# Kernel tuning notes

Measured on AMD Instinct MI355X. Metric: run time of the kernel, lower is better.

Reference implementation:

```python
import jax, jax.numpy as jnp
import numpy as np
import math
from itertools import permutations

B, C_IN, C_OUT, K, N, D, F_DIM = 2, 4, 8, 4, 224, 2, 128


def _make_perms(k):
    # [k!, k, k] permutation matrices, same ordering as itertools.permutations
    nP = math.factorial(k)
    perms = np.zeros((nP, k, k), dtype=np.float32)
    for c, p in enumerate(permutations(range(k))):
        perms[c, np.arange(k), np.array(p)] = 1.0
    return jnp.asarray(perms)


def setup_inputs() -> dict:
    key = jax.random.key(0)
    ks = jax.random.split(key, 6)
    graph = jax.random.normal(ks[0], (B, C_IN, N, N), jnp.float32)
    types = jax.random.normal(ks[1], (B, C_IN, N), jnp.float32)
    features = jax.random.normal(ks[2], (B, N, F_DIM), jnp.float32)
    # xavier-uniform-ish scales for the learned kernels
    k_struct = jax.random.normal(ks[3], (C_OUT, C_IN, K, K), jnp.float32) * 0.3
    k_row = jax.random.normal(ks[4], (C_OUT, C_IN, K), jnp.float32) * 0.5
    k_col = jax.random.normal(ks[5], (C_OUT, C_IN, K), jnp.float32) * 0.5
    return {"graph": graph, "types": types, "features": features,
            "k_struct": k_struct, "k_row": k_row, "k_col": k_col}


def _forward(graph, types, features, k_struct, k_row, k_col):
    Bn, C, Nn, _ = graph.shape
    k = k_struct.shape[-1]
    new_k = (k - 1) * D + 1
    nH = Nn - new_k + 1            # square graph -> nW == nH
    n_sub = nH * nH
    idx = jnp.arange(nH)[:, None] + jnp.arange(k) * D  # [nH, k] dilated window indices

    # --- _prepare: dilated subgraph extraction (vectorized gather) ---
    g = graph[:, :, idx, :]            # [B,C,nH,k,N]
    g = g[..., idx]                    # [B,C,nH,k,nH,k]
    sub = jnp.transpose(g, (0, 2, 4, 1, 3, 5)).reshape(Bn, n_sub, C, k, k)
    rt = jnp.transpose(types[:, :, idx], (0, 2, 1, 3))  # [B,nH,C,k]
    row_t = jnp.broadcast_to(rt[:, :, None], (Bn, nH, nH, C, k)).reshape(Bn, n_sub, C, k)
    col_t = jnp.broadcast_to(rt[:, None, :], (Bn, nH, nH, C, k)).reshape(Bn, n_sub, C, k)
    rf = features[:, idx, :].sum(axis=-2)              # [B,nH,F]
    feats = rf[:, :, None, :] + rf[:, None, :, :]      # row_features + col_features
    h_mean = feats.reshape(Bn, n_sub, -1).mean(axis=1)  # [B,F]

    # --- permuted kernels ---
    perms = _make_perms(k)                                  # [P,k,k]
    Kp = jnp.einsum('pau,oiuv,pbv->oipab', perms, k_struct, perms)  # P K P^T
    Rp = jnp.einsum('pau,oiu->oipa', perms, k_row)
    Cp = jnp.einsum('pau,oiu->oipa', perms, k_col)

    subf = sub.reshape(-1, C, k, k)   # [n,i,a,b], n = B*n_sub
    rtf = row_t.reshape(-1, C, k)
    ctf = col_t.reshape(-1, C, k)

    # ||X - Y||_F^2 = ||X||^2 + ||Y||^2 - 2<X,Y>, avoids the huge broadcasted diff
    def sq_dist(x2_ni, y2_opi, cross_nopi):
        return y2_opi[None] + x2_ni[:, None, None, :] - 2.0 * cross_nopi

    G2 = jnp.sum(subf * subf, axis=(-2, -1))                       # [n,i]
    K2 = jnp.transpose(jnp.sum(Kp * Kp, axis=(-2, -1)), (0, 2, 1))  # [o,p,i]
    struct = sq_dist(G2, K2, jnp.einsum('niab,oipab->nopi', subf, Kp))
    R2 = jnp.transpose(jnp.sum(Rp * Rp, axis=-1), (0, 2, 1))
    rsim = sq_dist(jnp.sum(rtf * rtf, axis=-1), R2, jnp.einsum('nia,oipa->nopi', rtf, Rp))
    C2 = jnp.transpose(jnp.sum(Cp * Cp, axis=-1), (0, 2, 1))
    csim = sq_dist(jnp.sum(ctf * ctf, axis=-1), C2, jnp.einsum('nia,oipa->nopi', ctf, Cp))

    total = struct + rsim + csim            # [n, o, P, i]
    # maxpool over P of (-total), negated back == min over permutations of total
    pooled = jnp.min(total, axis=2)         # [n, o, i]
    sims = jnp.transpose(pooled.reshape(Bn, n_sub, -1), (0, 2, 1))  # [B, o*i, n_sub]
    out_sim = (1.0 - jax.nn.softmax(sims, axis=-1)) / sims.shape[-1]
    return h_mean, out_sim


def reference(graph, types, features, k_struct, k_row, k_col):
    return _forward(graph, types, features, k_struct, k_row, k_col)
```

## Files before the change

### kernel.cpp

```cpp
#include <hip/hip_runtime.h>
#include <hip/hip_bf16.h>

#define B_    2
#define CIN   4
#define COUT  8
#define KK    4
#define DD    2
#define NN    224
#define FDIM  128
#define NH    218
#define NSUB  (NH*NH)
#define NPERM 24
#define NROWS (B_*COUT*CIN)
#define NSUB4 (NSUB/4)
#define CH4   512
#define MB    ((NSUB4 + CH4 - 1) / CH4)
#define OG    2
#define NCH1  ((NSUB + 255) / 256)
#define NEGBIG (-3.4e38f)

__device__ static constexpr int PERM[NPERM][4] = {
  {0,1,2,3},{0,1,3,2},{0,2,1,3},{0,2,3,1},{0,3,1,2},{0,3,2,1},
  {1,0,2,3},{1,0,3,2},{1,2,0,3},{1,2,3,0},{1,3,0,2},{1,3,2,0},
  {2,0,1,3},{2,0,3,1},{2,1,0,3},{2,1,3,0},{2,3,0,1},{2,3,1,0},
  {3,0,1,2},{3,0,2,1},{3,1,0,2},{3,1,2,0},{3,2,0,1},{3,2,1,0}
};

__global__ __launch_bounds__(64) void hmean_kernel(const float* __restrict__ features,
                                                   float* __restrict__ out) {
  int bf = blockIdx.x;
  int b = bf / FDIM, f = bf - b * FDIM;
  int lane = threadIdx.x;
  const float* fb = features + (size_t)b * NN * FDIM + f;
  float acc = 0.f;
  for (int r = lane; r < NN; r += 64) {
    int w = 0;
#pragma unroll
    for (int a = 0; a < KK; ++a) {
      int i0 = r - a * DD;
      if (0 <= i0 && i0 < NH) w++;
    }
    acc += (float)w * fb[(size_t)r * FDIM];
  }
#pragma unroll
  for (int off = 32; off > 0; off >>= 1) acc += __shfl_down(acc, off, 64);
  if (lane == 0) out[bf] = acc * (2.0f / (float)NH);
}

__global__ __launch_bounds__(256, 4) void sims_kernel(
    const float* __restrict__ graph, const float* __restrict__ types,
    const float* __restrict__ ksA, const float* __restrict__ krA,
    const float* __restrict__ kcA, float* __restrict__ simsOut)
{
  __shared__ float ls[COUT * CIN * 16];
  __shared__ float lr[COUT * CIN * 4];
  __shared__ float lc[COUT * CIN * 4];
  __shared__ float lK2[COUT * CIN];
  int t = threadIdx.x;
  for (int i = t; i < COUT * CIN * 16; i += 256) ls[i] = ksA[i];
  for (int i = t; i < COUT * CIN * 4; i += 256) { lr[i] = krA[i]; lc[i] = kcA[i]; }
  __syncthreads();
  if (t < COUT * CIN) {
    float k2 = 0.f;
#pragma unroll
    for (int u = 0; u < 16; ++u) k2 += ls[t * 16 + u] * ls[t * 16 + u];
#pragma unroll
    for (int u = 0; u < 4; ++u) k2 += lr[t * 4 + u] * lr[t * 4 + u] + lc[t * 4 + u] * lc[t * 4 + u];
    lK2[t] = k2;
  }
  __syncthreads();

  int s = blockIdx.x * 256 + t;
  if (s >= NSUB) return;
  int yi  = blockIdx.y;
  int og  = yi >> 3;
  int bci = yi & 7;
  int b   = bci >> 2;
  int ci  = bci & 3;
  int ii  = s / NH;
  int jj  = s - ii * NH;

  const float* gi = graph + ((size_t)b * CIN + ci) * NN * NN;
  const float* ti = types + ((size_t)b * CIN + ci) * NN;

  float subv[16], rtv[4], ctv[4];
  float G2 = 0.f, T2r = 0.f, T2c = 0.f;
#pragma unroll
  for (int a = 0; a < KK; ++a) {
    const float* row = gi + (size_t)(ii + a * DD) * NN + jj;
#pragma unroll
    for (int bb = 0; bb < KK; ++bb) {
      float v = row[bb * DD];
      subv[a * 4 + bb] = v;
      G2 += v * v;
    }
    float rv = ti[ii + a * DD];
    float cv = ti[jj + a * DD];
    rtv[a] = rv; ctv[a] = cv;
    T2r += rv * rv; T2c += cv * cv;
  }
  float base0 = G2 + T2r + T2c;

#pragma unroll 1
  for (int oo = 0; oo < COUT / OG; ++oo) {
    int o = og * (COUT / OG) + oo;
    int oc = o * CIN + ci;
    float kS[16], kR[4], kC[4];
    {
      const float4* pS4 = (const float4*)(ls + oc * 16);
#pragma unroll
      for (int u = 0; u < 4; ++u) {
        float4 q = pS4[u];
        kS[u*4+0] = q.x; kS[u*4+1] = q.y; kS[u*4+2] = q.z; kS[u*4+3] = q.w;
      }
      float4 qr = *(const float4*)(lr + oc * 4);
      kR[0] = qr.x; kR[1] = qr.y; kR[2] = qr.z; kR[3] = qr.w;
      float4 qc = *(const float4*)(lc + oc * 4);
      kC[0] = qc.x; kC[1] = qc.y; kC[2] = qc.z; kC[3] = qc.w;
    }

    float A0[4], A1[4], A2[4], A3[4];
#pragma unroll
    for (int x = 0; x < 4; ++x) {
      float d = kS[x * 4 + x];
      A0[x] = subv[0]  * d + rtv[0] * kR[x] + ctv[0] * kC[x];
      A1[x] = subv[5]  * d + rtv[1] * kR[x] + ctv[1] * kC[x];
      A2[x] = subv[10] * d + rtv[2] * kR[x] + ctv[2] * kC[x];
      A3[x] = subv[15] * d + rtv[3] * kR[x] + ctv[3] * kC[x];
    }

    float pair01[16], pair23[16];
#pragma unroll
    for (int x = 0; x < 4; ++x)
#pragma unroll
      for (int y = 0; y < 4; ++y) {
        if (x == y) continue;
        pair01[x * 4 + y] = A0[x] + A1[y]
                          + subv[0*4+1] * kS[x*4+y] + subv[1*4+0] * kS[y*4+x];
        pair23[x * 4 + y] = A2[x] + A3[y]
                          + subv[2*4+3] * kS[x*4+y] + subv[3*4+2] * kS[y*4+x];
      }

    float maxcr = NEGBIG;
#pragma unroll
    for (int p = 0; p < NPERM; ++p) {
      const int p0 = PERM[p][0], p1 = PERM[p][1], p2 = PERM[p][2], p3 = PERM[p][3];
      float cr = pair01[p0 * 4 + p1] + pair23[p2 * 4 + p3];
      cr += subv[0*4+2] * kS[p0*4+p2];
      cr += subv[2*4+0] * kS[p2*4+p0];
      cr += subv[0*4+3] * kS[p0*4+p3];
      cr += subv[3*4+0] * kS[p3*4+p0];
      cr += subv[1*4+2] * kS[p1*4+p2];
      cr += subv[2*4+1] * kS[p2*4+p1];
      cr += subv[1*4+3] * kS[p1*4+p3];
      cr += subv[3*4+1] * kS[p3*4+p1];
      maxcr = fmaxf(maxcr, cr);
    }
    float best = base0 + lK2[oc] - 2.0f * maxcr;

    simsOut[(size_t)((b * COUT + o) * CIN + ci) * NSUB + s] = best;
  }
}

__global__ __launch_bounds__(256) void softmax_partial(const float* __restrict__ sims,
                                                       float* __restrict__ partial) {
  int ch = blockIdx.x, row = blockIdx.y;
  int base4 = ch * CH4;
  int n4 = NSUB4 - base4; if (n4 > CH4) n4 = CH4;
  const float4* rp = (const float4*)(sims + (size_t)row * NSUB) + base4;
  int t = threadIdx.x;
  int wave = t >> 6, lane = t & 63;

  float4 a0, a1;
  bool h0 = (t < n4), h1 = (t + 256 < n4);
  if (h0) a0 = rp[t];
  if (h1) a1 = rp[t + 256];

  float m = NEGBIG;
  if (h0) m = fmaxf(fmaxf(a0.x, a0.y), fmaxf(a0.z, a0.w));
  if (h1) m = fmaxf(m, fmaxf(fmaxf(a1.x, a1.y), fmaxf(a1.z, a1.w)));
#pragma unroll
  for (int off = 32; off > 0; off >>= 1) m = fmaxf(m, __shfl_down(m, off, 64));
  __shared__ float red[8];
  if (lane == 0) red[wave] = m;
  __syncthreads();
  float M = fmaxf(fmaxf(red[0], red[1]), fmaxf(red[2], red[3]));

  float e = 0.f;
  if (h0) e  = __expf(a0.x - M) + __expf(a0.y - M) + __expf(a0.z - M) + __expf(a0.w - M);
  if (h1) e += __expf(a1.x - M) + __expf(a1.y - M) + __expf(a1.z - M) + __expf(a1.w - M);
#pragma unroll
  for (int off = 32; off > 0; off >>= 1) e += __shfl_down(e, off, 64);
  if (lane == 0) red[4 + wave] = e;
  __syncthreads();
  if (t == 0) {
    int idx = (row * MB + ch) * 2;
    partial[idx] = M;
    partial[idx + 1] = red[4] + red[5] + red[6] + red[7];
  }
}

__global__ __launch_bounds__(256) void softmax_final(float* __restrict__ sims,
                                                     const float* __restrict__ partial) {
  int ch = blockIdx.x, row = blockIdx.y;
  int t = threadIdx.x;

  __shared__ float sM, sInv;
  if (t < 64) {
    const float* pp = partial + row * MB * 2;
    float m = NEGBIG, l = 0.f;
    if (t < MB) { m = pp[2 * t]; l = pp[2 * t + 1]; }
#pragma unroll
    for (int off = 32; off > 0; off >>= 1) {
      float m2 = __shfl_down(m, off, 64);
      float l2 = __shfl_down(l, off, 64);
      float M = fmaxf(m, m2);
      l = l * __expf(m - M) + l2 * __expf(m2 - M);
      m = M;
    }
    if (t == 0) { sM = m; sInv = 1.0f / l; }
  }
  __syncthreads();
  float M = sM, invS = sInv;

  int base4 = ch * CH4;
  int n4 = NSUB4 - base4; if (n4 > CH4) n4 = CH4;
  float4* rp = (float4*)(sims + (size_t)row * NSUB) + base4;
  const float scale = 1.0f / (float)NSUB;
  for (int i = t; i < n4; i += 256) {
    float4 v = rp[i];
    v.x = (1.0f - __expf(v.x - M) * invS) * scale;
    v.y = (1.0f - __expf(v.y - M) * invS) * scale;
    v.z = (1.0f - __expf(v.z - M) * invS) * scale;
    v.w = (1.0f - __expf(v.w - M) * invS) * scale;
    rp[i] = v;
  }
}

extern "C" void kernel_launch(void* const* d_in, const int* in_sizes, int n_in,
                              void* d_out, int out_size, void* d_ws, size_t ws_size,
                              hipStream_t stream) {
  const float* graph    = (const float*)d_in[0];
  const float* types    = (const float*)d_in[1];
  const float* features = (const float*)d_in[2];
  const float* ks       = (const float*)d_in[3];
  const float* kr       = (const float*)d_in[4];
  const float* kc       = (const float*)d_in[5];
  float* out  = (float*)d_out;
  float* sims = out + B_ * FDIM;

  float* partial = (float*)d_ws;

  hmean_kernel<<<B_ * FDIM, 64, 0, stream>>>(features, out);
  dim3 sgrid(NCH1, B_ * CIN * OG);
  sims_kernel<<<sgrid, 256, 0, stream>>>(graph, types, ks, kr, kc, sims);
  dim3 pgrid(MB, NROWS);
  softmax_partial<<<pgrid, 256, 0, stream>>>(sims, partial);
  softmax_final<<<pgrid, 256, 0, stream>>>(sims, partial);
}
```

Baseline: 106.6 us.

## Recast permutation similarity as bf16-split MFMA GEMM against permuted kernels

Builds a permuted-kernel matrix (24 perms x 8 outputs per input channel) in a prep kernel, stored as bf16 hi/lo pairs. The sims kernel treats each subgraph's 24 features as a GEMM row and runs three bf16 MFMAs (hi*hi, hi*lo, lo*hi) to approximate an fp32 dot product, then takes the max over permutations with a shuffle. This replaces the scalar FMA permutation enumeration with matrix-core work. In exchange it adds a launch, LDS staging and some precision loss from dropping the lo*lo term.

```diff
diff --git a/kernel.cpp b/kernel.cpp
--- a/kernel.cpp
+++ b/kernel.cpp
@@ -15,9 +15,15 @@
 #define NSUB4 (NSUB/4)
 #define CH4   512
 #define MB    ((NSUB4 + CH4 - 1) / CH4)
-#define OG    2
-#define NCH1  ((NSUB + 255) / 256)
 #define NEGBIG (-3.4e38f)
+#define NCOL  192
+#define MTILE 128
+#define NBLK  ((NSUB + MTILE - 1) / MTILE)
+#define STR   40
+
+typedef short short8 __attribute__((ext_vector_type(8)));
+typedef float f32x4 __attribute__((ext_vector_type(4)));
+typedef unsigned short ushort_t;
 
 __device__ static constexpr int PERM[NPERM][4] = {
   {0,1,2,3},{0,1,3,2},{0,2,1,3},{0,2,3,1},{0,3,1,2},{0,3,2,1},
@@ -25,6 +31,53 @@
   {2,0,1,3},{2,0,3,1},{2,1,0,3},{2,1,3,0},{2,3,0,1},{2,3,1,0},
   {3,0,1,2},{3,0,2,1},{3,1,0,2},{3,1,2,0},{3,2,0,1},{3,2,1,0}
 };
+
+__device__ __forceinline__ void bf16split(float v, ushort_t* h, ushort_t* l) {
+  __hip_bfloat16 hh = __float2bfloat16(v);
+  float hf = __bfloat162float(hh);
+  __hip_bfloat16 ll = __float2bfloat16(v - hf);
+  *h = *(const ushort_t*)&hh;
+  *l = *(const ushort_t*)&ll;
+}
+
+__global__ __launch_bounds__(256) void prep_kernel(
+    const float* __restrict__ ks, const float* __restrict__ kr,
+    const float* __restrict__ kc, ushort_t* __restrict__ BTgHi,
+    ushort_t* __restrict__ BTgLo, float* __restrict__ K2g)
+{
+  int t = threadIdx.x;
+  for (int idx = t; idx < CIN * NCOL; idx += 256) {
+    int ci = idx / NCOL, col = idx - ci * NCOL;
+    int p = col >> 3, o = col & 7;
+    int oc = o * CIN + ci;
+    const int* pr = PERM[p];
+    float vals[32];
+#pragma unroll
+    for (int a = 0; a < 4; ++a) {
+#pragma unroll
+      for (int bb = 0; bb < 4; ++bb)
+        vals[a * 4 + bb] = ks[oc * 16 + pr[a] * 4 + pr[bb]];
+      vals[16 + a] = kr[oc * 4 + pr[a]];
+      vals[20 + a] = kc[oc * 4 + pr[a]];
+    }
+#pragma unroll
+    for (int u = 24; u < 32; ++u) vals[u] = 0.f;
+    ushort_t* dh = BTgHi + idx * 32;
+    ushort_t* dl = BTgLo + idx * 32;
+#pragma unroll
+    for (int u = 0; u < 32; ++u) bf16split(vals[u], dh + u, dl + u);
+  }
+  if (t < 32) {
+    int ci = t >> 3, o = t & 7, oc = o * CIN + ci;
+    float s2 = 0.f;
+#pragma unroll
+    for (int u = 0; u < 16; ++u) s2 += ks[oc * 16 + u] * ks[oc * 16 + u];
+#pragma unroll
+    for (int u = 0; u < 4; ++u)
+      s2 += kr[oc * 4 + u] * kr[oc * 4 + u] + kc[oc * 4 + u] * kc[oc * 4 + u];
+    K2g[t] = s2;
+  }
+}
 
 __global__ __launch_bounds__(64) void hmean_kernel(const float* __restrict__ features,
                                                    float* __restrict__ out) {
@@ -47,118 +100,127 @@
   if (lane == 0) out[bf] = acc * (2.0f / (float)NH);
 }
 
-__global__ __launch_bounds__(256, 4) void sims_kernel(
+__global__ __launch_bounds__(256, 2) void sims_mfma_kernel(
     const float* __restrict__ graph, const float* __restrict__ types,
-    const float* __restrict__ ksA, const float* __restrict__ krA,
-    const float* __restrict__ kcA, float* __restrict__ simsOut)
+    const ushort_t* __restrict__ BTgHi, const ushort_t* __restrict__ BTgLo,
+    const float* __restrict__ K2g, float* __restrict__ simsOut)
 {
-  __shared__ float ls[COUT * CIN * 16];
-  __shared__ float lr[COUT * CIN * 4];
-  __shared__ float lc[COUT * CIN * 4];
-  __shared__ float lK2[COUT * CIN];
+  __shared__ ushort_t lsAhi[MTILE * STR];
+  __shared__ ushort_t lsAlo[MTILE * STR];
+  __shared__ ushort_t lsBThi[NCOL * STR];
+  __shared__ ushort_t lsBTlo[NCOL * STR];
+  __shared__ float lsBase[MTILE];
+  __shared__ float lsK2[8];
+
   int t = threadIdx.x;
-  for (int i = t; i < COUT * CIN * 16; i += 256) ls[i] = ksA[i];
-  for (int i = t; i < COUT * CIN * 4; i += 256) { lr[i] = krA[i]; lc[i] = kcA[i]; }
-  __syncthreads();
-  if (t < COUT * CIN) {
-    float k2 = 0.f;
-#pragma unroll
-    for (int u = 0; u < 16; ++u) k2 += ls[t * 16 + u] * ls[t * 16 + u];
-#pragma unroll
-    for (int u = 0; u < 4; ++u) k2 += lr[t * 4 + u] * lr[t * 4 + u] + lc[t * 4 + u] * lc[t * 4 + u];
-    lK2[t] = k2;
-  }
-  __syncthreads();
-
-  int s = blockIdx.x * 256 + t;
-  if (s >= NSUB) return;
-  int yi  = blockIdx.y;
-  int og  = yi >> 3;
-  int bci = yi & 7;
-  int b   = bci >> 2;
-  int ci  = bci & 3;
-  int ii  = s / NH;
-  int jj  = s - ii * NH;
-
-  const float* gi = graph + ((size_t)b * CIN + ci) * NN * NN;
-  const float* ti = types + ((size_t)b * CIN + ci) * NN;
-
-  float subv[16], rtv[4], ctv[4];
-  float G2 = 0.f, T2r = 0.f, T2c = 0.f;
-#pragma unroll
-  for (int a = 0; a < KK; ++a) {
-    const float* row = gi + (size_t)(ii + a * DD) * NN + jj;
-#pragma unroll
-    for (int bb = 0; bb < KK; ++bb) {
-      float v = row[bb * DD];
-      subv[a * 4 + bb] = v;
-      G2 += v * v;
-    }
-    float rv = ti[ii + a * DD];
-    float cv = ti[jj + a * DD];
-    rtv[a] = rv; ctv[a] = cv;
-    T2r += rv * rv; T2c += cv * cv;
-  }
-  float base0 = G2 + T2r + T2c;
+  int s_base = blockIdx.x * MTILE;
+  int b = blockIdx.y;
+  int wv = t >> 6, lane = t & 63;
+  int c16 = lane & 15, quad = lane >> 4;
 
 #pragma unroll 1
-  for (int oo = 0; oo < COUT / OG; ++oo) {
-    int o = og * (COUT / OG) + oo;
-    int oc = o * CIN + ci;
-    float kS[16], kR[4], kC[4];
-    {
-      const float4* pS4 = (const float4*)(ls + oc * 16);
-#pragma unroll
-      for (int u = 0; u < 4; ++u) {
-        float4 q = pS4[u];
-        kS[u*4+0] = q.x; kS[u*4+1] = q.y; kS[u*4+2] = q.z; kS[u*4+3] = q.w;
-      }
-      float4 qr = *(const float4*)(lr + oc * 4);
-      kR[0] = qr.x; kR[1] = qr.y; kR[2] = qr.z; kR[3] = qr.w;
-      float4 qc = *(const float4*)(lc + oc * 4);
-      kC[0] = qc.x; kC[1] = qc.y; kC[2] = qc.z; kC[3] = qc.w;
-    }
-
-    float A0[4], A1[4], A2[4], A3[4];
-#pragma unroll
-    for (int x = 0; x < 4; ++x) {
-      float d = kS[x * 4 + x];
-      A0[x] = subv[0]  * d + rtv[0] * kR[x] + ctv[0] * kC[x];
-      A1[x] = subv[5]  * d + rtv[1] * kR[x] + ctv[1] * kC[x];
-      A2[x] = subv[10] * d + rtv[2] * kR[x] + ctv[2] * kC[x];
-      A3[x] = subv[15] * d + rtv[3] * kR[x] + ctv[3] * kC[x];
-    }
-
-    float pair01[16], pair23[16];
-#pragma unroll
-    for (int x = 0; x < 4; ++x)
-#pragma unroll
-      for (int y = 0; y < 4; ++y) {
-        if (x == y) continue;
-        pair01[x * 4 + y] = A0[x] + A1[y]
-                          + subv[0*4+1] * kS[x*4+y] + subv[1*4+0] * kS[y*4+x];
-        pair23[x * 4 + y] = A2[x] + A3[y]
-                          + subv[2*4+3] * kS[x*4+y] + subv[3*4+2] * kS[y*4+x];
-      }
-
-    float maxcr = NEGBIG;
-#pragma unroll
-    for (int p = 0; p < NPERM; ++p) {
-      const int p0 = PERM[p][0], p1 = PERM[p][1], p2 = PERM[p][2], p3 = PERM[p][3];
-      float cr = pair01[p0 * 4 + p1] + pair23[p2 * 4 + p3];
-      cr += subv[0*4+2] * kS[p0*4+p2];
-      cr += subv[2*4+0] * kS[p2*4+p0];
-      cr += subv[0*4+3] * kS[p0*4+p3];
-      cr += subv[3*4+0] * kS[p3*4+p0];
-      cr += subv[1*4+2] * kS[p1*4+p2];
-      cr += subv[2*4+1] * kS[p2*4+p1];
-      cr += subv[1*4+3] * kS[p1*4+p3];
-      cr += subv[3*4+1] * kS[p3*4+p1];
-      maxcr = fmaxf(maxcr, cr);
-    }
-    float best = base0 + lK2[oc] - 2.0f * maxcr;
-
-    simsOut[(size_t)((b * COUT + o) * CIN + ci) * NSUB + s] = best;
+  for (int ci = 0; ci < CIN; ++ci) {
+    __syncthreads();
+    if (t < 128) {
+      int r = t;
+      int s = s_base + r;
+      float xv[24];
+      if (s < NSUB) {
+        int ii = s / NH, jj = s - ii * NH;
+        const float* gi = graph + (size_t)(b * CIN + ci) * NN * NN;
+        const float* ti = types + (size_t)(b * CIN + ci) * NN;
+        float bsum = 0.f;
+#pragma unroll
+        for (int a = 0; a < 4; ++a) {
+          const float* row = gi + (size_t)(ii + a * DD) * NN + jj;
+#pragma unroll
+          for (int bb = 0; bb < 4; ++bb) {
+            float v = row[bb * DD];
+            xv[a * 4 + bb] = v;
+            bsum += v * v;
+          }
+          float rv = ti[ii + a * DD];
+          float cv = ti[jj + a * DD];
+          xv[16 + a] = rv; xv[20 + a] = cv;
+          bsum += rv * rv + cv * cv;
+        }
+        lsBase[r] = bsum;
+      } else {
+#pragma unroll
+        for (int u = 0; u < 24; ++u) xv[u] = 0.f;
+        lsBase[r] = 0.f;
+      }
+      ushort_t* ah = lsAhi + r * STR;
+      ushort_t* al = lsAlo + r * STR;
+#pragma unroll
+      for (int u = 0; u < 24; ++u) bf16split(xv[u], ah + u, al + u);
+#pragma unroll
+      for (int u = 24; u < 32; ++u) { ah[u] = 0; al[u] = 0; }
+      if (t < 8) lsK2[t] = K2g[ci * 8 + t];
+    } else {
+      int tt = t - 128;
+      const ushort_t* srcH = BTgHi + ci * (NCOL * 32);
+      const ushort_t* srcL = BTgLo + ci * (NCOL * 32);
+#pragma unroll
+      for (int i = tt; i < NCOL * 4; i += 128) {
+        int col = i >> 2, part = i & 3;
+        *(short8*)(lsBThi + col * STR + part * 8) = *(const short8*)(srcH + i * 8);
+        *(short8*)(lsBTlo + col * STR + part * 8) = *(const short8*)(srcL + i * 8);
+      }
+    }
+    __syncthreads();
+
+    float mx[2][4];
+#pragma unroll
+    for (int m2 = 0; m2 < 2; ++m2)
+#pragma unroll
+      for (int rr = 0; rr < 4; ++rr) mx[m2][rr] = NEGBIG;
+
+#pragma unroll 1
+    for (int half = 0; half < 2; ++half) {
+      short8 bh[6], bl[6];
+#pragma unroll
+      for (int j = 0; j < 6; ++j) {
+        int col = (half * 6 + j) * 16 + c16;
+        bh[j] = *(const short8*)(lsBThi + col * STR + quad * 8);
+        bl[j] = *(const short8*)(lsBTlo + col * STR + quad * 8);
+      }
+#pragma unroll
+      for (int m2 = 0; m2 < 2; ++m2) {
+        int mt = wv * 2 + m2;
+        int arow = mt * 16 + c16;
+        short8 ah = *(const short8*)(lsAhi + arow * STR + quad * 8);
+        short8 al = *(const short8*)(lsAlo + arow * STR + quad * 8);
+#pragma unroll
+        for (int j = 0; j < 6; ++j) {
+          f32x4 c = {0.f, 0.f, 0.f, 0.f};
+          c = __builtin_amdgcn_mfma_f32_16x16x32_bf16(ah, bh[j], c, 0, 0, 0);
+          c = __builtin_amdgcn_mfma_f32_16x16x32_bf16(ah, bl[j], c, 0, 0, 0);
+          c = __builtin_amdgcn_mfma_f32_16x16x32_bf16(al, bh[j], c, 0, 0, 0);
+#pragma unroll
+          for (int rr = 0; rr < 4; ++rr) mx[m2][rr] = fmaxf(mx[m2][rr], c[rr]);
+        }
+      }
+    }
+
+    int o = lane & 7;
+    float k2o = lsK2[o];
+    bool writer = (lane & 8) == 0;
+#pragma unroll
+    for (int m2 = 0; m2 < 2; ++m2) {
+      int mt = wv * 2 + m2;
+#pragma unroll
+      for (int rr = 0; rr < 4; ++rr) {
+        float v = mx[m2][rr];
+        v = fmaxf(v, __shfl_xor(v, 8, 64));
+        int m = mt * 16 + quad * 4 + rr;
+        int s = s_base + m;
+        if (writer && s < NSUB) {
+          float val = lsBase[m] + k2o - 2.0f * v;
+          simsOut[(size_t)((b * COUT + o) * CIN + ci) * NSUB + s] = val;
+        }
+      }
+    }
   }
 }
 
@@ -249,11 +311,15 @@
   float* out  = (float*)d_out;
   float* sims = out + B_ * FDIM;
 
-  float* partial = (float*)d_ws;
-
+  float* partial  = (float*)d_ws;
+  ushort_t* BTgHi = (ushort_t*)((char*)d_ws + 16384);
+  ushort_t* BTgLo = (ushort_t*)((char*)d_ws + 16384 + 49152);
+  float* K2g      = (float*)((char*)d_ws + 16384 + 2 * 49152);
+
+  prep_kernel<<<1, 256, 0, stream>>>(ks, kr, kc, BTgHi, BTgLo, K2g);
   hmean_kernel<<<B_ * FDIM, 64, 0, stream>>>(features, out);
-  dim3 sgrid(NCH1, B_ * CIN * OG);
-  sims_kernel<<<sgrid, 256, 0, stream>>>(graph, types, ks, kr, kc, sims);
+  dim3 ggrid(NBLK, B_);
+  sims_mfma_kernel<<<ggrid, 256, 0, stream>>>(graph, types, BTgHi, BTgLo, K2g, sims);
   dim3 pgrid(MB, NROWS);
   softmax_partial<<<pgrid, 256, 0, stream>>>(sims, partial);
   softmax_final<<<pgrid, 256, 0, stream>>>(sims, partial);
```

Result: no change. 106.8 us (+0.1%).
